# Kernel tuning notes

Measured on AMD Instinct MI355X. Metric: run time of the kernel, lower is better.

The kernel has to match this reference:

```python
import jax, jax.numpy as jnp
import numpy as np
import math

B, N, H, NH, HD, G = 2, 1024, 512, 8, 64, 50
MAX_DIST = 10.0


def setup_inputs() -> dict:
    key = jax.random.key(0)
    ks = jax.random.split(key, 12)
    s = 0.02  # small init scale for weights
    return {
        'x': jax.random.normal(ks[0], (B, N, H), jnp.float32),
        'distances': jax.random.uniform(ks[1], (B, N, N), jnp.float32) * MAX_DIST,
        'mask': jnp.ones((B, N), jnp.int32),
        'widths': jnp.ones((G,), jnp.float32) * 0.5,
        'dp_w': jax.random.normal(ks[2], (G, NH), jnp.float32) * s,
        'dp_b': jnp.zeros((NH,), jnp.float32),
        'wq': jax.random.normal(ks[3], (H, H), jnp.float32) * s,
        'bq': jnp.zeros((H,), jnp.float32),
        'wk': jax.random.normal(ks[4], (H, H), jnp.float32) * s,
        'bk': jnp.zeros((H,), jnp.float32),
        'wv': jax.random.normal(ks[5], (H, H), jnp.float32) * s,
        'bv': jnp.zeros((H,), jnp.float32),
        'wo': jax.random.normal(ks[6], (H, H), jnp.float32) * s,
        'bo': jnp.zeros((H,), jnp.float32),
        'ln1_g': jnp.ones((H,), jnp.float32),
        'ln1_b': jnp.zeros((H,), jnp.float32),
        'ln2_g': jnp.ones((H,), jnp.float32),
        'ln2_b': jnp.zeros((H,), jnp.float32),
        'w1': jax.random.normal(ks[7], (H, 4 * H), jnp.float32) * s,
        'b1': jnp.zeros((4 * H,), jnp.float32),
        'w2': jax.random.normal(ks[8], (4 * H, H), jnp.float32) * s,
        'b2': jnp.zeros((H,), jnp.float32),
    }


def _layernorm(x, g, b, eps=1e-5):
    mu = jnp.mean(x, axis=-1, keepdims=True)
    var = jnp.mean(jnp.square(x - mu), axis=-1, keepdims=True)
    return (x - mu) * jax.lax.rsqrt(var + eps) * g + b


def reference(x, distances, mask, widths, dp_w, dp_b, wq, bq, wk, bk, wv, bv,
              wo, bo, ln1_g, ln1_b, ln2_g, ln2_b, w1, b1, w2, b2):
    centers = jnp.linspace(0.0, MAX_DIST, G, dtype=jnp.float32)  # buffer

    residual = x
    xn = _layernorm(x, ln1_g, ln1_b)

    def split_heads(t):  # [B,N,H] -> [B,NH,N,HD]
        return t.reshape(B, N, NH, HD).transpose(0, 2, 1, 3)

    q = split_heads(xn @ wq + bq)
    k = split_heads(xn @ wk + bk)
    v = split_heads(xn @ wv + bv)

    scores = jnp.einsum('bhqd,bhkd->bhqk', q, k) / math.sqrt(HD)

    # Gaussian distance encoding: [B,N,N,G]
    diff = distances[..., None] - centers
    gf = jnp.exp(-jnp.square(diff) / (2.0 * jnp.square(widths)))
    # project to per-head bias, then permute to [B,NH,N,N]
    dist_bias = (gf @ dp_w + dp_b).transpose(0, 3, 1, 2)
    scores = scores + dist_bias

    key_mask = mask[:, None, None, :]  # [B,1,1,N]
    scores = jnp.where(key_mask == 0, -1e9, scores)

    attn = jax.nn.softmax(scores, axis=-1)
    out = jnp.einsum('bhqk,bhkd->bhqd', attn, v)
    out = out.transpose(0, 2, 1, 3).reshape(B, N, H)
    out = out @ wo + bo

    x = residual + out
    residual = x
    xn = _layernorm(x, ln2_g, ln2_b)
    h = jax.nn.gelu(xn @ w1 + b1, approximate=False)  # dropout is identity in eval
    x = residual + (h @ w2 + b2)
    return x
```

## Files before the change

kernel.cpp:

```cpp
#include <hip/hip_runtime.h>
#include <hip/hip_bf16.h>
#include <math.h>

#define B_ 2
#define N_ 1024
#define H_ 512
#define NH_ 8
#define HD_ 64
#define G_ 50
#define TAB_ 1024
constexpr float MAXD = 10.0f;

typedef __attribute__((ext_vector_type(8))) short short8;
typedef __attribute__((ext_vector_type(4))) float f32x4;

__device__ inline ushort f2bf(float v) {
  __hip_bfloat16 h = __float2bfloat16(v);
  return *(ushort*)&h;
}
__device__ inline float bf2f(ushort u) {
  unsigned x = ((unsigned)u) << 16;
  return __uint_as_float(x);
}
__device__ inline void gload_lds16(const ushort* g, ushort* l) {
  __builtin_amdgcn_global_load_lds(
      (const __attribute__((address_space(1))) void*)g,
      (__attribute__((address_space(3))) void*)l, 16, 0, 0);
}

__global__ __launch_bounds__(128) void ln_k(const float* __restrict__ x,
                                            const float* __restrict__ g,
                                            const float* __restrict__ b,
                                            ushort* __restrict__ out) {
  int row = blockIdx.x;
  const float* xr = x + (size_t)row * H_;
  int t = threadIdx.x;
  float4 v = *(const float4*)(xr + t * 4);
  float s = v.x + v.y + v.z + v.w;
  float sq = v.x * v.x + v.y * v.y + v.z * v.z + v.w * v.w;
  #pragma unroll
  for (int m = 1; m < 64; m <<= 1) {
    s += __shfl_xor(s, m, 64);
    sq += __shfl_xor(sq, m, 64);
  }
  __shared__ float red[2][2];
  int wid = t >> 6;
  if ((t & 63) == 0) { red[wid][0] = s; red[wid][1] = sq; }
  __syncthreads();
  s = red[0][0] + red[1][0];
  sq = red[0][1] + red[1][1];
  float mu = s * (1.0f / H_);
  float var = sq * (1.0f / H_) - mu * mu;
  float rs = rsqrtf(var + 1e-5f);
  float4 gg = *(const float4*)(g + t * 4);
  float4 bb = *(const float4*)(b + t * 4);
  ushort4 o;
  o.x = f2bf((v.x - mu) * rs * gg.x + bb.x);
  o.y = f2bf((v.y - mu) * rs * gg.y + bb.y);
  o.z = f2bf((v.z - mu) * rs * gg.z + bb.z);
  o.w = f2bf((v.w - mu) * rs * gg.w + bb.w);
  *(ushort4*)(out + (size_t)row * H_ + t * 4) = o;
}

__device__ inline void transp_dev(const float* __restrict__ src,
                                  ushort* __restrict__ d, int R, int C,
                                  int bx, int by, int t, float (*tile)[33]) {
  int r0 = by * 32, c0 = bx * 32;
  int rr = t >> 5, cc = t & 31;
  #pragma unroll
  for (int p = 0; p < 4; ++p)
    tile[rr + p * 8][cc] = src[(size_t)(r0 + rr + p * 8) * C + c0 + cc];
  __syncthreads();
  #pragma unroll
  for (int p = 0; p < 4; ++p)
    d[(size_t)(c0 + rr + p * 8) * R + r0 + cc] = f2bf(tile[cc][rr + p * 8]);
}

__global__ __launch_bounds__(256) void prep_k(
    const float* wq, const float* wk, const float* wv, const float* wo,
    const float* w1, const float* w2, ushort* __restrict__ wT4,
    ushort* __restrict__ w1T, ushort* __restrict__ w2T,
    const float* __restrict__ widths, const float* __restrict__ dp_w,
    const float* __restrict__ dp_b, float2* __restrict__ tab2) {
  __shared__ float tile[32][33];
  int bid = blockIdx.x, t = threadIdx.x;
  if (bid < 1024) {
    int z = bid >> 8, rem = bid & 255;
    const float* src = (z == 0) ? wq : (z == 1) ? wk : (z == 2) ? wv : wo;
    transp_dev(src, wT4 + (size_t)z * 512 * 512, 512, 512, rem & 15, rem >> 4, t, tile);
  } else if (bid < 2048) {
    int rem = bid - 1024;
    transp_dev(w1, w1T, 512, 2048, rem & 63, rem >> 6, t, tile);
  } else if (bid < 3072) {
    int rem = bid - 2048;
    transp_dev(w2, w2T, 2048, 512, rem & 15, rem >> 4, t, tile);
  } else {
    int i = (bid - 3072) * 256 + t;
    if (i >= NH_ * (TAB_ + 1)) return;
    int h = i / (TAB_ + 1), tt = i % (TAB_ + 1);
    int t1 = tt < TAB_ ? tt + 1 : tt;
    float d0 = (float)tt * (MAXD / TAB_);
    float d1 = (float)t1 * (MAXD / TAB_);
    float v0 = dp_b[h], v1 = dp_b[h];
    for (int g = 0; g < G_; ++g) {
      float c = (float)g * (MAXD / 49.0f);
      float w = widths[g];
      float inv = -1.0f / (2.0f * w * w);
      float wg = dp_w[g * NH_ + h];
      float e0 = d0 - c, e1 = d1 - c;
      v0 += expf(e0 * e0 * inv) * wg;
      v1 += expf(e1 * e1 * inv) * wg;
    }
    tab2[i] = make_float2(v0, v1);
  }
}

enum { EPI_QKV = 1, EPI_RES = 2, EPI_GELU = 3, EPI_PART = 4 };

template <int BM, int BN, int EPI>
__global__ __launch_bounds__(256) void mfma_gemm(const ushort* __restrict__ A,
                                                 const ushort* __restrict__ Bt,
                                                 const float* __restrict__ b0,
                                                 const float* __restrict__ b1,
                                                 const float* __restrict__ b2,
                                                 const float* __restrict__ resid,
                                                 void* __restrict__ outv,
                                                 int K, int Ks, int Nc) {
  __shared__ ushort As[2][BM * 32];
  __shared__ ushort Bs[2][BN * 32];
  int t = threadIdx.x;
  int z = blockIdx.z;
  const ushort* Bz;
  int k0;
  if constexpr (EPI == EPI_PART) {
    Bz = Bt;
    k0 = z * K;
  } else {
    Bz = Bt + (size_t)z * Nc * Ks;
    k0 = 0;
  }
  const float* bias = (z == 0) ? b0 : (z == 1) ? b1 : b2;
  int m0 = blockIdx.y * BM, n0 = blockIdx.x * BN;
  int lane = t & 63, w = t >> 6, wr = w >> 1, wc = w & 1;
  int lrow = lane & 15, lkg = lane >> 4;
  constexpr int NFM = BM / 32, NFN = BN / 32;
  constexpr int AL = BM / 64, BL = BN / 64;
  f32x4 acc[NFM][NFN] = {};
  int rl = lane >> 2, kgl = lane & 3;

  auto stage = [&](int buf, int kt) {
    #pragma unroll
    for (int p = 0; p < AL; ++p) {
      int r = w * (BM / 4) + p * 16 + rl;
      int kgs = kgl ^ (r & 3);
      gload_lds16(&A[(size_t)(m0 + r) * Ks + k0 + kt + kgs * 8],
                  &As[buf][(w * (BM / 4) + p * 16) * 32]);
    }
    #pragma unroll
    for (int p = 0; p < BL; ++p) {
      int r = w * (BN / 4) + p * 16 + rl;
      int kgs = kgl ^ (r & 3);
      gload_lds16(&Bz[(size_t)(n0 + r) * Ks + k0 + kt + kgs * 8],
                  &Bs[buf][(w * (BN / 4) + p * 16) * 32]);
    }
  };
  auto compute = [&](int buf) {
    short8 af[NFM], bfr[NFN];
    #pragma unroll
    for (int fm = 0; fm < NFM; ++fm) {
      int r = wr * (BM / 2) + fm * 16 + lrow;
      af[fm] = *(const short8*)&As[buf][r * 32 + ((lkg ^ (r & 3)) << 3)];
    }
    #pragma unroll
    for (int fn = 0; fn < NFN; ++fn) {
      int r = wc * (BN / 2) + fn * 16 + lrow;
      bfr[fn] = *(const short8*)&Bs[buf][r * 32 + ((lkg ^ (r & 3)) << 3)];
    }
    #pragma unroll
    for (int fm = 0; fm < NFM; ++fm)
      #pragma unroll
      for (int fn = 0; fn < NFN; ++fn)
        acc[fm][fn] = __builtin_amdgcn_mfma_f32_16x16x32_bf16(af[fm], bfr[fn],
                                                              acc[fm][fn], 0, 0, 0);
  };

  stage(0, 0);
  __syncthreads();
  int cur = 0;
  for (int kt = 0; kt < K; kt += 32) {
    if (kt + 32 < K) stage(cur ^ 1, kt + 32);
    compute(cur);
    __syncthreads();
    cur ^= 1;
  }

  int rbase = (lane >> 4) * 4;
  #pragma unroll
  for (int fm = 0; fm < NFM; ++fm) {
    #pragma unroll
    for (int fn = 0; fn < NFN; ++fn) {
      #pragma unroll
      for (int j = 0; j < 4; ++j) {
        int row = m0 + wr * (BM / 2) + fm * 16 + rbase + j;
        int col = n0 + wc * (BN / 2) + fn * 16 + lrow;
        if constexpr (EPI == EPI_PART) {
          size_t M = (size_t)gridDim.y * BM;
          ((float*)outv)[(size_t)z * M * Nc + (size_t)row * Nc + col] =
              acc[fm][fn][j];
        } else {
          float v = acc[fm][fn][j] + bias[col];
          if constexpr (EPI == EPI_QKV) {
            ushort* q = (ushort*)outv + (size_t)z * (1 << 20);
            int bb = row >> 10, n = row & (N_ - 1);
            int h = col >> 6, d = col & 63;
            if (z < 2)
              q[(((size_t)(bb * NH_ + h)) * N_ + n) * HD_ + d] = f2bf(v);
            else
              q[(((size_t)(bb * NH_ + h)) * HD_ + d) * N_ + n] = f2bf(v);
          } else if constexpr (EPI == EPI_RES) {
            ((float*)outv)[(size_t)row * Nc + col] =
                resid[(size_t)row * Nc + col] + v;
          } else {
            ((ushort*)outv)[(size_t)row * Nc + col] =
                f2bf(0.5f * v * (1.0f + erff(v * 0.70710678118654752f)));
          }
        }
      }
    }
  }
}

__global__ __launch_bounds__(256) void comb2_k(const float* __restrict__ p,
                                               const float* __restrict__ resid,
                                               const float* __restrict__ bias,
                                               float* __restrict__ out) {
  int idx = blockIdx.x * 256 + threadIdx.x;
  int base = idx * 4;
  int col = base & (H_ - 1);
  f32x4 a = *(const f32x4*)&p[base];
  f32x4 b = *(const f32x4*)&p[(1 << 20) + base];
  f32x4 r = *(const f32x4*)&resid[base];
  f32x4 bi = *(const f32x4*)&bias[col];
  f32x4 o = r + a + b + bi;
  *(f32x4*)&out[base] = o;
}

__global__ __launch_bounds__(128) void comb2ln_k(const float* __restrict__ p,
                                                 const float* __restrict__ resid,
                                                 const float* __restrict__ bias,
                                                 const float* __restrict__ g,
                                                 const float* __restrict__ bl,
                                                 float* __restrict__ x1out,
                                                 ushort* __restrict__ xnout) {
  int row = blockIdx.x, t = threadIdx.x;
  int base = row * H_ + t * 4;
  f32x4 a = *(const f32x4*)&p[base];
  f32x4 b2v = *(const f32x4*)&p[(1 << 20) + base];
  f32x4 r = *(const f32x4*)&resid[base];
  f32x4 bi = *(const f32x4*)&bias[t * 4];
  f32x4 v = r + a + b2v + bi;
  *(f32x4*)&x1out[base] = v;
  float s = v[0] + v[1] + v[2] + v[3];
  float sq = v[0] * v[0] + v[1] * v[1] + v[2] * v[2] + v[3] * v[3];
  #pragma unroll
  for (int m = 1; m < 64; m <<= 1) {
    s += __shfl_xor(s, m, 64);
    sq += __shfl_xor(sq, m, 64);
  }
  __shared__ float red[2][2];
  int wid = t >> 6;
  if ((t & 63) == 0) { red[wid][0] = s; red[wid][1] = sq; }
  __syncthreads();
  s = red[0][0] + red[1][0];
  sq = red[0][1] + red[1][1];
  float mu = s * (1.0f / H_);
  float var = sq * (1.0f / H_) - mu * mu;
  float rs = rsqrtf(var + 1e-5f);
  float4 gg = *(const float4*)(g + t * 4);
  float4 bb = *(const float4*)(bl + t * 4);
  ushort4 o;
  o.x = f2bf((v[0] - mu) * rs * gg.x + bb.x);
  o.y = f2bf((v[1] - mu) * rs * gg.y + bb.y);
  o.z = f2bf((v[2] - mu) * rs * gg.z + bb.z);
  o.w = f2bf((v[3] - mu) * rs * gg.w + bb.w);
  *(ushort4*)(xnout + (size_t)row * H_ + t * 4) = o;
}

constexpr int QT = 64, KT = 64, NJH = 2, NTH = N_ / (KT * NJH);
constexpr int JH = N_ / NJH;

__global__ __launch_bounds__(256) void attn_k(
    const ushort* __restrict__ q, const ushort* __restrict__ k,
    const ushort* __restrict__ v, const float* __restrict__ dist,
    const int* __restrict__ mask, const float2* __restrict__ tab2g,
    float* __restrict__ Op, float2* __restrict__ ml) {
  int qt = blockIdx.x, h = blockIdx.y, z = blockIdx.z;
  int b = z >> 1, jh = z & 1;
  int i0 = qt * QT;
  int jbase = jh * JH;
  __shared__ ushort Ks[KT * 64];
  __shared__ ushort Vt[64 * KT];
  __shared__ ushort Bsb[QT * 68];
  __shared__ ushort Ps[4][16 * 64];
  __shared__ float2 tl2[TAB_ + 1];
  __shared__ float mfl[JH];
  int t = threadIdx.x;
  int lane = t & 63, w = t >> 6;
  int l = lane & 15, g = lane >> 4;

  for (int i = t; i <= TAB_; i += 256) tl2[i] = tab2g[h * (TAB_ + 1) + i];
  for (int i = t; i < JH; i += 256) mfl[i] = (mask[b * N_ + jbase + i] == 0) ? -1e9f : 0.0f;

  const size_t ho = ((size_t)(b * NH_ + h)) * N_ * HD_;
  const ushort* qb = q + ho;
  const ushort* kb = k + ho;
  const ushort* vb = v + ho;

  int qrow = i0 + w * 16 + l;
  short8 qf[2];
  qf[0] = *(const short8*)&qb[(size_t)qrow * 64 + g * 8];
  qf[1] = *(const short8*)&qb[(size_t)qrow * 64 + 32 + g * 8];

  int c2 = t & 7, jr = t >> 3;
  int dr_r = t >> 2, dr_c = (t & 3) * 16;

  auto stK = [&](short8 val, int j2) {
    *(short8*)&Ks[j2 * 64 + ((c2 ^ (j2 & 7)) << 3)] = val;
  };
  auto stV = [&](short8 val, int d) {
    *(short8*)&Vt[d * 64 + ((c2 ^ (d & 7)) << 3)] = val;
  };

  short8 k0a, k1a, v0a, v1a;
  f32x4 dda[4];
  {
    const ushort* kn = kb + (size_t)jbase * 64;
    const ushort* vn = vb + jbase;
    k0a = *(const short8*)&kn[(size_t)jr * 64 + c2 * 8];
    k1a = *(const short8*)&kn[(size_t)(jr + 32) * 64 + c2 * 8];
    v0a = *(const short8*)&vn[(size_t)jr * N_ + c2 * 8];
    v1a = *(const short8*)&vn[(size_t)(jr + 32) * N_ + c2 * 8];
    const float* db = dist + ((size_t)b * N_ + (i0 + dr_r)) * N_ + jbase + dr_c;
    #pragma unroll
    for (int p = 0; p < 4; ++p) dda[p] = *(const f32x4*)&db[p * 4];
  }
  __syncthreads();
  {
    stK(k0a, jr); stK(k1a, jr + 32);
    stV(v0a, jr); stV(v1a, jr + 32);
    #pragma unroll
    for (int p = 0; p < 4; ++p) {
      ushort4 ov;
      #pragma unroll
      for (int e = 0; e < 4; ++e) {
        int jcol = dr_c + p * 4 + e;
        float u = dda[p][e] * ((float)TAB_ / MAXD);
        int it = (int)u;
        it = it < 0 ? 0 : (it > TAB_ - 1 ? TAB_ - 1 : it);
        float f = u - (float)it;
        float2 tv = tl2[it];
        ((ushort*)&ov)[e] = f2bf(tv.x + f * (tv.y - tv.x) + mfl[jcol]);
      }
      *(ushort4*)&Bsb[dr_r * 68 + dr_c + p * 4] = ov;
    }
  }
  __syncthreads();

  float m_[4] = {-1e30f, -1e30f, -1e30f, -1e30f};
  float l_[4] = {0.f, 0.f, 0.f, 0.f};
  f32x4 acc[4] = {{0,0,0,0},{0,0,0,0},{0,0,0,0},{0,0,0,0}};

  for (int tt = 0; tt < NTH; ++tt) {
    const int j0 = jbase + tt * KT;
    if (tt + 1 < NTH) {
      const ushort* kn = kb + (size_t)(j0 + KT) * 64;
      const ushort* vn = vb + (j0 + KT);
      k0a = *(const short8*)&kn[(size_t)jr * 64 + c2 * 8];
      k1a = *(const short8*)&kn[(size_t)(jr + 32) * 64 + c2 * 8];
      v0a = *(const short8*)&vn[(size_t)jr * N_ + c2 * 8];
      v1a = *(const short8*)&vn[(size_t)(jr + 32) * N_ + c2 * 8];
      const float* db = dist + ((size_t)b * N_ + (i0 + dr_r)) * N_ + j0 + KT + dr_c;
      #pragma unroll
      for (int p = 0; p < 4; ++p) dda[p] = *(const f32x4*)&db[p * 4];
    }
    f32x4 sa[4] = {{0,0,0,0},{0,0,0,0},{0,0,0,0},{0,0,0,0}};
    __builtin_amdgcn_s_setprio(1);
    #pragma unroll
    for (int dblk = 0; dblk < 2; ++dblk)
      #pragma unroll
      for (int fj = 0; fj < 4; ++fj) {
        int j2 = fj * 16 + l;
        short8 kf = *(const short8*)&Ks[j2 * 64 + (((dblk * 4 + g) ^ (j2 & 7)) << 3)];
        sa[fj] = __builtin_amdgcn_mfma_f32_16x16x32_bf16(qf[dblk], kf, sa[fj], 0, 0, 0);
      }
    __builtin_amdgcn_s_setprio(0);
    float al_[4];
    int qloc = w * 16 + 4 * g;
    #pragma unroll
    for (int reg = 0; reg < 4; ++reg) {
      float svr[4];
      #pragma unroll
      for (int fj = 0; fj < 4; ++fj)
        svr[fj] = fmaf(sa[fj][reg], 0.125f,
                       bf2f(Bsb[(qloc + reg) * 68 + fj * 16 + l]));
      float rm = fmaxf(fmaxf(svr[0], svr[1]), fmaxf(svr[2], svr[3]));
      rm = fmaxf(rm, __shfl_xor(rm, 1, 64));
      rm = fmaxf(rm, __shfl_xor(rm, 2, 64));
      rm = fmaxf(rm, __shfl_xor(rm, 4, 64));
      rm = fmaxf(rm, __shfl_xor(rm, 8, 64));
      float mn = fmaxf(m_[reg], rm);
      float al = __expf(m_[reg] - mn);
      m_[reg] = mn;
      al_[reg] = al;
      float ps = 0.f;
      int qlq = 4 * g + reg;
      #pragma unroll
      for (int fj = 0; fj < 4; ++fj) {
        float p = __expf(svr[fj] - mn);
        ps += p;
        int c = fj * 2 + (l >> 3);
        Ps[w][qlq * 64 + ((c ^ (qlq & 7)) << 3) + (l & 7)] = f2bf(p);
      }
      ps += __shfl_xor(ps, 1, 64);
      ps += __shfl_xor(ps, 2, 64);
      ps += __shfl_xor(ps, 4, 64);
      ps += __shfl_xor(ps, 8, 64);
      l_[reg] = l_[reg] * al + ps;
    }
    #pragma unroll
    for (int fd = 0; fd < 4; ++fd)
      #pragma unroll
      for (int reg = 0; reg < 4; ++reg) acc[fd][reg] *= al_[reg];
    __builtin_amdgcn_s_setprio(1);
    #pragma unroll
    for (int jj = 0; jj < 2; ++jj) {
      short8 pa = *(const short8*)&Ps[w][l * 64 + (((jj * 4 + g) ^ (l & 7)) << 3)];
      #pragma unroll
      for (int fd = 0; fd < 4; ++fd) {
        int d2 = fd * 16 + l;
        short8 vf = *(const short8*)&Vt[d2 * 64 + (((jj * 4 + g) ^ (d2 & 7)) << 3)];
        acc[fd] = __builtin_amdgcn_mfma_f32_16x16x32_bf16(pa, vf, acc[fd], 0, 0, 0);
      }
    }
    __builtin_amdgcn_s_setprio(0);
    __syncthreads();
    if (tt + 1 < NTH) {
      stK(k0a, jr); stK(k1a, jr + 32);
      stV(v0a, jr); stV(v1a, jr + 32);
      const int jloc = (tt + 1) * KT;
      #pragma unroll
      for (int p = 0; p < 4; ++p) {
        ushort4 ov;
        #pragma unroll
        for (int e = 0; e < 4; ++e) {
          int jcol = dr_c + p * 4 + e;
          float u = dda[p][e] * ((float)TAB_ / MAXD);
          int it = (int)u;
          it = it < 0 ? 0 : (it > TAB_ - 1 ? TAB_ - 1 : it);
          float f = u - (float)it;
          float2 tv = tl2[it];
          ((ushort*)&ov)[e] = f2bf(tv.x + f * (tv.y - tv.x) + mfl[jloc + jcol]);
        }
        *(ushort4*)&Bsb[dr_r * 68 + dr_c + p * 4] = ov;
      }
    }
    __syncthreads();
  }
  const size_t pbase = (((size_t)(b * NJH + jh) * NH_ + h) * N_) + i0;
  #pragma unroll
  for (int reg = 0; reg < 4; ++reg) {
    int rowl = w * 16 + 4 * g + reg;
    float* op = Op + (pbase + rowl) * HD_ + l;
    #pragma unroll
    for (int fd = 0; fd < 4; ++fd) op[fd * 16] = acc[fd][reg];
    if (l == 0) ml[pbase + rowl] = make_float2(m_[reg], l_[reg]);
  }
}

__global__ __launch_bounds__(256) void comb_k(const float* __restrict__ Op,
                                              const float2* __restrict__ ml,
                                              ushort* __restrict__ ao) {
  int idx = blockIdx.x * 256 + threadIdx.x;
  int row = idx >> 4;
  int dq = (idx & 15) * 4;
  int b = row >> 13, h = (row >> 10) & 7, n = row & 1023;
  size_t p0 = (((size_t)(b * NJH + 0) * NH_ + h) * N_) + n;
  size_t p1 = (((size_t)(b * NJH + 1) * NH_ + h) * N_) + n;
  float2 v0 = ml[p0], v1 = ml[p1];
  float M = fmaxf(v0.x, v1.x);
  float a0 = __expf(v0.x - M), a1 = __expf(v1.x - M);
  float inv = 1.0f / (v0.y * a0 + v1.y * a1);
  float4 O0 = *(const float4*)&Op[p0 * HD_ + dq];
  float4 O1 = *(const float4*)&Op[p1 * HD_ + dq];
  ushort4 o;
  o.x = f2bf((O0.x * a0 + O1.x * a1) * inv);
  o.y = f2bf((O0.y * a0 + O1.y * a1) * inv);
  o.z = f2bf((O0.z * a0 + O1.z * a1) * inv);
  o.w = f2bf((O0.w * a0 + O1.w * a1) * inv);
  *(ushort4*)&ao[((size_t)(b * N_ + n)) * H_ + h * HD_ + dq] = o;
}

extern "C" void kernel_launch(void* const* d_in, const int* in_sizes, int n_in,
                              void* d_out, int out_size, void* d_ws, size_t ws_size,
                              hipStream_t stream) {
  const float* x = (const float*)d_in[0];
  const float* distances = (const float*)d_in[1];
  const int* mask = (const int*)d_in[2];
  const float* widths = (const float*)d_in[3];
  const float* dp_w = (const float*)d_in[4];
  const float* dp_b = (const float*)d_in[5];
  const float* wq = (const float*)d_in[6];
  const float* bq = (const float*)d_in[7];
  const float* wk = (const float*)d_in[8];
  const float* bk = (const float*)d_in[9];
  const float* wv = (const float*)d_in[10];
  const float* bv = (const float*)d_in[11];
  const float* wo = (const float*)d_in[12];
  const float* bo = (const float*)d_in[13];
  const float* ln1_g = (const float*)d_in[14];
  const float* ln1_b = (const float*)d_in[15];
  const float* ln2_g = (const float*)d_in[16];
  const float* ln2_b = (const float*)d_in[17];
  const float* w1 = (const float*)d_in[18];
  const float* b1 = (const float*)d_in[19];
  const float* w2 = (const float*)d_in[20];
  const float* b2 = (const float*)d_in[21];
  float* out = (float*)d_out;
  float* wsf = (float*)d_ws;

  const size_t M1 = (size_t)1 << 20;
  ushort* qkvb = (ushort*)wsf;
  float* x1 = wsf + 2 * M1;
  ushort* hbuf = (ushort*)(wsf + 3 * M1);
  ushort* xn = (ushort*)(wsf + 5 * M1);
  ushort* xn2 = (ushort*)(wsf + 5 * M1 + M1 / 2);
  ushort* ao = (ushort*)(wsf + 6 * M1);
  ushort* wT4 = (ushort*)(wsf + 6 * M1 + M1 / 2);
  ushort* w1T = (ushort*)(wsf + 7 * M1);
  ushort* w2T = (ushort*)(wsf + 7 * M1 + M1 / 2);
  float2* tab2 = (float2*)(wsf + 8 * M1);
  float* Op = wsf + 9 * M1;
  float2* ml = (float2*)(wsf + 11 * M1);
  float* pAO = wsf + 12 * M1;
  float* pF2 = wsf + 14 * M1;

  prep_k<<<3105, 256, 0, stream>>>(wq, wk, wv, wo, w1, w2, wT4, w1T, w2T,
                                   widths, dp_w, dp_b, tab2);

  ln_k<<<B_ * N_, 128, 0, stream>>>(x, ln1_g, ln1_b, xn);

  mfma_gemm<64, 64, EPI_QKV><<<dim3(8, 32, 3), 256, 0, stream>>>(
      xn, wT4, bq, bk, bv, nullptr, qkvb, 512, 512, 512);

  attn_k<<<dim3(N_ / QT, NH_, B_ * NJH), 256, 0, stream>>>(
      qkvb, qkvb + M1, qkvb + 2 * M1, distances, mask, tab2, Op, ml);
  comb_k<<<1024, 256, 0, stream>>>(Op, ml, ao);

  mfma_gemm<64, 64, EPI_PART><<<dim3(8, 32, 2), 256, 0, stream>>>(
      ao, wT4 + (size_t)3 * 512 * 512, bo, bo, bo, nullptr, pAO, 256, 512, 512);
  comb2ln_k<<<B_ * N_, 128, 0, stream>>>(pAO, x, bo, ln2_g, ln2_b, x1, xn2);

  mfma_gemm<128, 64, EPI_GELU><<<dim3(32, 16, 1), 256, 0, stream>>>(
      xn2, w1T, b1, b1, b1, nullptr, hbuf, 512, 512, 2048);

  mfma_gemm<64, 64, EPI_PART><<<dim3(8, 32, 2), 256, 0, stream>>>(
      hbuf, w2T, b2, b2, b2, nullptr, pF2, 1024, 2048, 512);
  comb2_k<<<1024, 256, 0, stream>>>(pF2, x1, b2, out);
}
```

Baseline: 106.3 us.

## Double-buffer attention K/V/bias tiles and fold first layernorm into prep kernel

The attention kernel now keeps two LDS buffers for the K, V and distance-bias tiles. The next tile is written into the alternate buffer while the current one is consumed, which removes one __syncthreads per iteration. The standalone layernorm launch is merged into the weight-prep kernel as extra blocks handling two rows each, saving a kernel launch. The cost is higher LDS use in attention, which may lower occupancy.

```diff
diff --git a/kernel.cpp b/kernel.cpp
--- a/kernel.cpp
+++ b/kernel.cpp
@@ -26,40 +26,6 @@
   __builtin_amdgcn_global_load_lds(
       (const __attribute__((address_space(1))) void*)g,
       (__attribute__((address_space(3))) void*)l, 16, 0, 0);
-}
-
-__global__ __launch_bounds__(128) void ln_k(const float* __restrict__ x,
-                                            const float* __restrict__ g,
-                                            const float* __restrict__ b,
-                                            ushort* __restrict__ out) {
-  int row = blockIdx.x;
-  const float* xr = x + (size_t)row * H_;
-  int t = threadIdx.x;
-  float4 v = *(const float4*)(xr + t * 4);
-  float s = v.x + v.y + v.z + v.w;
-  float sq = v.x * v.x + v.y * v.y + v.z * v.z + v.w * v.w;
-  #pragma unroll
-  for (int m = 1; m < 64; m <<= 1) {
-    s += __shfl_xor(s, m, 64);
-    sq += __shfl_xor(sq, m, 64);
-  }
-  __shared__ float red[2][2];
-  int wid = t >> 6;
-  if ((t & 63) == 0) { red[wid][0] = s; red[wid][1] = sq; }
-  __syncthreads();
-  s = red[0][0] + red[1][0];
-  sq = red[0][1] + red[1][1];
-  float mu = s * (1.0f / H_);
-  float var = sq * (1.0f / H_) - mu * mu;
-  float rs = rsqrtf(var + 1e-5f);
-  float4 gg = *(const float4*)(g + t * 4);
-  float4 bb = *(const float4*)(b + t * 4);
-  ushort4 o;
-  o.x = f2bf((v.x - mu) * rs * gg.x + bb.x);
-  o.y = f2bf((v.y - mu) * rs * gg.y + bb.y);
-  o.z = f2bf((v.z - mu) * rs * gg.z + bb.z);
-  o.w = f2bf((v.w - mu) * rs * gg.w + bb.w);
-  *(ushort4*)(out + (size_t)row * H_ + t * 4) = o;
 }
 
 __device__ inline void transp_dev(const float* __restrict__ src,
@@ -81,8 +47,11 @@
     const float* w1, const float* w2, ushort* __restrict__ wT4,
     ushort* __restrict__ w1T, ushort* __restrict__ w2T,
     const float* __restrict__ widths, const float* __restrict__ dp_w,
-    const float* __restrict__ dp_b, float2* __restrict__ tab2) {
+    const float* __restrict__ dp_b, float2* __restrict__ tab2,
+    const float* __restrict__ x, const float* __restrict__ ln1g,
+    const float* __restrict__ ln1b, ushort* __restrict__ xn) {
   __shared__ float tile[32][33];
+  __shared__ float red2[4][2];
   int bid = blockIdx.x, t = threadIdx.x;
   if (bid < 1024) {
     int z = bid >> 8, rem = bid & 255;
@@ -94,7 +63,7 @@
   } else if (bid < 3072) {
     int rem = bid - 2048;
     transp_dev(w2, w2T, 2048, 512, rem & 15, rem >> 4, t, tile);
-  } else {
+  } else if (bid < 3105) {
     int i = (bid - 3072) * 256 + t;
     if (i >= NH_ * (TAB_ + 1)) return;
     int h = i / (TAB_ + 1), tt = i % (TAB_ + 1);
@@ -112,6 +81,34 @@
       v1 += expf(e1 * e1 * inv) * wg;
     }
     tab2[i] = make_float2(v0, v1);
+  } else {
+    int row = (bid - 3105) * 2 + (t >> 7);
+    int tl = t & 127;
+    float4 v = *(const float4*)(x + (size_t)row * H_ + tl * 4);
+    float s = v.x + v.y + v.z + v.w;
+    float sq = v.x * v.x + v.y * v.y + v.z * v.z + v.w * v.w;
+    #pragma unroll
+    for (int m = 1; m < 64; m <<= 1) {
+      s += __shfl_xor(s, m, 64);
+      sq += __shfl_xor(sq, m, 64);
+    }
+    int wid = t >> 6;
+    if ((t & 63) == 0) { red2[wid][0] = s; red2[wid][1] = sq; }
+    __syncthreads();
+    int rw = (t >> 7) * 2;
+    s = red2[rw][0] + red2[rw + 1][0];
+    sq = red2[rw][1] + red2[rw + 1][1];
+    float mu = s * (1.0f / H_);
+    float var = sq * (1.0f / H_) - mu * mu;
+    float rs = rsqrtf(var + 1e-5f);
+    float4 gg = *(const float4*)(ln1g + tl * 4);
+    float4 bb = *(const float4*)(ln1b + tl * 4);
+    ushort4 o;
+    o.x = f2bf((v.x - mu) * rs * gg.x + bb.x);
+    o.y = f2bf((v.y - mu) * rs * gg.y + bb.y);
+    o.z = f2bf((v.z - mu) * rs * gg.z + bb.z);
+    o.w = f2bf((v.w - mu) * rs * gg.w + bb.w);
+    *(ushort4*)(xn + (size_t)row * H_ + tl * 4) = o;
   }
 }
 
@@ -298,9 +295,9 @@
   int b = z >> 1, jh = z & 1;
   int i0 = qt * QT;
   int jbase = jh * JH;
-  __shared__ ushort Ks[KT * 64];
-  __shared__ ushort Vt[64 * KT];
-  __shared__ ushort Bsb[QT * 68];
+  __shared__ ushort Ks[2][KT * 64];
+  __shared__ ushort Vt[2][64 * KT];
+  __shared__ ushort Bsb[2][QT * 68];
   __shared__ ushort Ps[4][16 * 64];
   __shared__ float2 tl2[TAB_ + 1];
   __shared__ float mfl[JH];
@@ -324,11 +321,11 @@
   int c2 = t & 7, jr = t >> 3;
   int dr_r = t >> 2, dr_c = (t & 3) * 16;
 
-  auto stK = [&](short8 val, int j2) {
-    *(short8*)&Ks[j2 * 64 + ((c2 ^ (j2 & 7)) << 3)] = val;
+  auto stK = [&](int buf, short8 val, int j2) {
+    *(short8*)&Ks[buf][j2 * 64 + ((c2 ^ (j2 & 7)) << 3)] = val;
   };
-  auto stV = [&](short8 val, int d) {
-    *(short8*)&Vt[d * 64 + ((c2 ^ (d & 7)) << 3)] = val;
+  auto stV = [&](int buf, short8 val, int d) {
+    *(short8*)&Vt[buf][d * 64 + ((c2 ^ (d & 7)) << 3)] = val;
   };
 
   short8 k0a, k1a, v0a, v1a;
@@ -346,8 +343,8 @@
   }
   __syncthreads();
   {
-    stK(k0a, jr); stK(k1a, jr + 32);
-    stV(v0a, jr); stV(v1a, jr + 32);
+    stK(0, k0a, jr); stK(0, k1a, jr + 32);
+    stV(0, v0a, jr); stV(0, v1a, jr + 32);
     #pragma unroll
     for (int p = 0; p < 4; ++p) {
       ushort4 ov;
@@ -361,7 +358,7 @@
         float2 tv = tl2[it];
         ((ushort*)&ov)[e] = f2bf(tv.x + f * (tv.y - tv.x) + mfl[jcol]);
       }
-      *(ushort4*)&Bsb[dr_r * 68 + dr_c + p * 4] = ov;
+      *(ushort4*)&Bsb[0][dr_r * 68 + dr_c + p * 4] = ov;
     }
   }
   __syncthreads();
@@ -370,6 +367,7 @@
   float l_[4] = {0.f, 0.f, 0.f, 0.f};
   f32x4 acc[4] = {{0,0,0,0},{0,0,0,0},{0,0,0,0},{0,0,0,0}};
 
+  int cur = 0;
   for (int tt = 0; tt < NTH; ++tt) {
     const int j0 = jbase + tt * KT;
     if (tt + 1 < NTH) {
@@ -390,7 +388,7 @@
       #pragma unroll
       for (int fj = 0; fj < 4; ++fj) {
         int j2 = fj * 16 + l;
-        short8 kf = *(const short8*)&Ks[j2 * 64 + (((dblk * 4 + g) ^ (j2 & 7)) << 3)];
+        short8 kf = *(const short8*)&Ks[cur][j2 * 64 + (((dblk * 4 + g) ^ (j2 & 7)) << 3)];
         sa[fj] = __builtin_amdgcn_mfma_f32_16x16x32_bf16(qf[dblk], kf, sa[fj], 0, 0, 0);
       }
     __builtin_amdgcn_s_setprio(0);
@@ -402,7 +400,7 @@
       #pragma unroll
       for (int fj = 0; fj < 4; ++fj)
         svr[fj] = fmaf(sa[fj][reg], 0.125f,
-                       bf2f(Bsb[(qloc + reg) * 68 + fj * 16 + l]));
+                       bf2f(Bsb[cur][(qloc + reg) * 68 + fj * 16 + l]));
       float rm = fmaxf(fmaxf(svr[0], svr[1]), fmaxf(svr[2], svr[3]));
       rm = fmaxf(rm, __shfl_xor(rm, 1, 64));
       rm = fmaxf(rm, __shfl_xor(rm, 2, 64));
@@ -438,15 +436,15 @@
       #pragma unroll
       for (int fd = 0; fd < 4; ++fd) {
         int d2 = fd * 16 + l;
-        short8 vf = *(const short8*)&Vt[d2 * 64 + (((jj * 4 + g) ^ (d2 & 7)) << 3)];
+        short8 vf = *(const short8*)&Vt[cur][d2 * 64 + (((jj * 4 + g) ^ (d2 & 7)) << 3)];
         acc[fd] = __builtin_amdgcn_mfma_f32_16x16x32_bf16(pa, vf, acc[fd], 0, 0, 0);
       }
     }
     __builtin_amdgcn_s_setprio(0);
-    __syncthreads();
     if (tt + 1 < NTH) {
-      stK(k0a, jr); stK(k1a, jr + 32);
-      stV(v0a, jr); stV(v1a, jr + 32);
+      int nb = cur ^ 1;
+      stK(nb, k0a, jr); stK(nb, k1a, jr + 32);
+      stV(nb, v0a, jr); stV(nb, v1a, jr + 32);
       const int jloc = (tt + 1) * KT;
       #pragma unroll
       for (int p = 0; p < 4; ++p) {
@@ -461,10 +459,11 @@
           float2 tv = tl2[it];
           ((ushort*)&ov)[e] = f2bf(tv.x + f * (tv.y - tv.x) + mfl[jloc + jcol]);
         }
-        *(ushort4*)&Bsb[dr_r * 68 + dr_c + p * 4] = ov;
+        *(ushort4*)&Bsb[nb][dr_r * 68 + dr_c + p * 4] = ov;
       }
     }
     __syncthreads();
+    cur ^= 1;
   }
   const size_t pbase = (((size_t)(b * NJH + jh) * NH_ + h) * N_) + i0;
   #pragma unroll
@@ -544,10 +543,8 @@
   float* pAO = wsf + 12 * M1;
   float* pF2 = wsf + 14 * M1;
 
-  prep_k<<<3105, 256, 0, stream>>>(wq, wk, wv, wo, w1, w2, wT4, w1T, w2T,
-                                   widths, dp_w, dp_b, tab2);
-
-  ln_k<<<B_ * N_, 128, 0, stream>>>(x, ln1_g, ln1_b, xn);
+  prep_k<<<4129, 256, 0, stream>>>(wq, wk, wv, wo, w1, w2, wT4, w1T, w2T,
+                                   widths, dp_w, dp_b, tab2, x, ln1_g, ln1_b, xn);
 
   mfma_gemm<64, 64, EPI_QKV><<<dim3(8, 32, 3), 256, 0, stream>>>(
       xn, wT4, bq, bk, bv, nullptr, qkvb, 512, 512, 512);
```

Result: faster. 103.5 us (-2.6%).
